# Performance work log

Measured on AMD Instinct MI355X. Metric: run time of the kernel, lower is better.

Reference implementation:

```python
import jax, jax.numpy as jnp
import numpy as np
import math

HEADS = 8
DIM_HEAD = 64
BATCH = 2
SEQ = 2048
KNN = 32
ATTN_SCALE_INIT = 20.0


def l2norm(t, eps=1e-12):
    n = jnp.sqrt(jnp.sum(t * t, axis=-1, keepdims=True))
    return t / jnp.maximum(n, eps)


def setup_inputs() -> dict:
    key = jax.random.key(0)
    ks = jax.random.split(key, 5)
    q = jax.random.normal(ks[0], (BATCH, HEADS, SEQ, DIM_HEAD), dtype=jnp.float32)
    k = jax.random.normal(ks[1], (BATCH, SEQ, DIM_HEAD), dtype=jnp.float32)
    v = jax.random.normal(ks[2], (BATCH, SEQ, DIM_HEAD), dtype=jnp.float32)
    scale_param = jnp.full((HEADS, 1, 1), math.log(ATTN_SCALE_INIT), dtype=jnp.float32)
    mem_kv = jax.random.normal(ks[3], (BATCH, HEADS, SEQ, KNN, 2, DIM_HEAD), dtype=jnp.float32)
    mask = jnp.ones((BATCH, SEQ), dtype=jnp.float32)
    mem_mask = jax.random.randint(ks[4], (BATCH, HEADS, SEQ, KNN), 0, 2).astype(jnp.bool_)
    return {"q": q, "k": k, "v": v, "scale_param": scale_param,
            "mem_kv": mem_kv, "mask": mask, "mem_mask": mem_mask}


def reference(q, k, v, scale_param, mem_kv, mask, mem_mask):
    neg = -jnp.finfo(q.dtype).max
    qn = l2norm(q)
    kn = l2norm(k)
    scale = jnp.exp(scale_param)  # [h,1,1]

    # local attention scores: [b,h,i,j]
    sim = jnp.einsum('bhid,bjd->bhij', qn, kn) * scale
    # key padding mask
    sim = sim + neg * (1.0 - mask[:, None, None, :])
    # causal mask (use_causal_mask=True), i == j here
    i, j = sim.shape[-2], sim.shape[-1]
    causal = jnp.triu(jnp.ones((i, j), dtype=jnp.bool_), j - i + 1)
    sim = jnp.where(causal, neg, sim)

    # memory branch: mem_kv [b,h,i,knn,2,d]
    mem_k = mem_kv[..., 0, :]
    mem_v = mem_kv[..., 1, :]
    sim_mem = jnp.einsum('bhid,bhijd->bhij', qn, mem_k) * scale
    sim_mem = jnp.where(mem_mask, sim_mem, neg)

    # joint softmax over [mem | local]
    full = jnp.concatenate((sim_mem, sim), axis=-1)
    attn = jax.nn.softmax(full, axis=-1)

    knn = mem_mask.shape[-1]
    mem_attn = attn[..., :knn]
    local_attn = attn[..., knn:]

    local_out = jnp.einsum('bhij,bjd->bhid', local_attn, v)
    mem_out = jnp.einsum('bhij,bhijd->bhid', mem_attn, mem_v)
    return local_out + mem_out
```

## Files before the change

### kernel.cpp

```cpp
#include <hip/hip_runtime.h>
#include <float.h>

#define HEADS 8
#define DIM 64
#define BATCH 2
#define SEQ 2048
#define KNN 32
#define QT 32
#define KT 64
#define NEGF (-3.402823466e38f)

typedef float f32x4 __attribute__((ext_vector_type(4)));
typedef __bf16 bf16x8 __attribute__((ext_vector_type(8)));

union F4 { float4 v; f32x4 e; float f[4]; };
union S8 { bf16x8 b; unsigned int u[4]; unsigned short us[8]; uint4 u4; uint2 u2[2]; };

__device__ __forceinline__ unsigned short f2bf(float x) {
    unsigned int u = __float_as_uint(x);
    u = (u + 0x7fffu + ((u >> 16) & 1u)) >> 16;
    return (unsigned short)u;
}


__global__ __launch_bounds__(256) void prep_kernel(const float* __restrict__ k,
                                                   const float* __restrict__ v,
                                                   const unsigned char* __restrict__ mmraw,
                                                   unsigned short* __restrict__ knBt,
                                                   unsigned short* __restrict__ vTt,
                                                   int* __restrict__ flag) {
    __shared__ float kn_s[64][65];
    __shared__ float vt_s[64][65];
    const int w = threadIdx.x >> 6, lane = threadIdx.x & 63;
    const int s0 = blockIdx.x * 64;
    const int b = s0 >> 11;
    const int s64 = (s0 & 2047) >> 6;
    for (int rr = 0; rr < 16; rr++) {
        const int sl = w * 16 + rr;
        const int row = s0 + sl;
        float kv = k[(size_t)row * DIM + lane];
        float ssq = kv * kv;
        #pragma unroll
        for (int m = 1; m < 64; m <<= 1) ssq += __shfl_xor(ssq, m);
        kn_s[sl][lane] = kv / fmaxf(sqrtf(ssq), 1e-12f);
        vt_s[sl][lane] = v[(size_t)row * DIM + lane];
    }
    __syncthreads();
    #pragma unroll
    for (int i = 0; i < 2; i++) {
        const int ch = threadIdx.x * 2 + i;
        const int s16g = ch >> 7;
        const int rem = ch & 127;
        const int rowc = rem >> 3;
        const int kc = (rem >> 2) & 1;
        const int oct = rem & 3;
        const float* src = &kn_s[s16g * 16 + rowc][kc * 32 + oct * 8];
        unsigned short tmp[8];
        #pragma unroll
        for (int e = 0; e < 8; e++) tmp[e] = f2bf(src[e]);
        const int s16 = s64 * 4 + s16g;
        unsigned short* dst = knBt + (((size_t)(b * 128 + s16) * 2 + kc) << 9)
                            + rowc * 32 + oct * 8;
        *(uint4*)dst = *(uint4*)&tmp[0];
    }
    #pragma unroll
    for (int i = 0; i < 2; i++) {
        const int ch = threadIdx.x * 2 + i;
        const int kk2 = ch >> 8;
        const int mtd = (ch >> 6) & 3;
        const int cc = (ch >> 2) & 15;
        const int q = ch & 3;
        unsigned short tmp[8];
        #pragma unroll
        for (int e = 0; e < 8; e++)
            tmp[e] = f2bf(vt_s[kk2 * 32 + q * 8 + e][mtd * 16 + cc]);
        unsigned short* dst = vTt + (((size_t)(b * 32 + s64) * 8 + kk2 * 4 + mtd) << 9)
                            + cc * 32 + q * 8;
        *(uint4*)dst = *(uint4*)&tmp[0];
    }
    if (blockIdx.x == 0 && w == 0) {
        int bad = 0;
        #pragma unroll
        for (int t = 0; t < 8; t++) {
            int idx = t * 64 + lane;
            if ((idx & 3) != 0 && mmraw[idx] != 0) bad = 1;
        }
        unsigned long long anybad = __ballot(bad);
        if (lane == 0) flag[0] = (anybad == 0ULL) ? 1 : 0;
    }
}

__global__ __launch_bounds__(256, 4) void mem_kernel(
    const float* __restrict__ q,
    const float* __restrict__ scale_param,
    const float* __restrict__ mem_kv,
    const void*  __restrict__ mem_mask,
    const int*   __restrict__ flagp,
    unsigned short* __restrict__ qnB,
    float* __restrict__ maccG,
    float* __restrict__ mG,
    float* __restrict__ lG)
{
    __shared__ float qn_s[4][64];
    __shared__ float p_s[4][32];
    const int w = threadIdx.x >> 6, lane = threadIdx.x & 63;
    const int mask_is_int = flagp[0];
    const int gid = blockIdx.x * 4 + w;
    const float scale = __expf(scale_param[(gid >> 11) & 7]);
    const float* rowp = mem_kv + (size_t)gid * (KNN * 2 * DIM);

    const int j1 = lane & 31, dh = lane >> 5;
    bool mybit;
    {
        size_t mmrow = (size_t)gid * KNN;
        mybit = mask_is_int ? (((const int*)mem_mask)[mmrow + j1] != 0)
                            : (((const unsigned char*)mem_mask)[mmrow + j1] != 0);
    }
    const unsigned int mb = (unsigned int)__ballot(mybit);

    float qv = q[(size_t)gid * DIM + lane];

    F4 dk[8];
    #pragma unroll
    for (int i = 0; i < 8; i++) dk[i].e = 0.f;
    {
        const float* kbase = rowp + j1 * (2 * DIM) + dh * 32;
        if (mybit) {
            #pragma unroll
            for (int i = 0; i < 8; i++) dk[i].e = *(const f32x4*)(kbase + 4 * i);
        }
    }
    const int g = lane >> 4, c16 = lane & 15;
    F4 dv[8];
    #pragma unroll
    for (int t = 0; t < 8; t++) {
        dv[t].e = 0.f;
        const int j2 = 4 * t + g;
        if ((mb >> j2) & 1u)
            dv[t].e = *(const f32x4*)(rowp + j2 * (2 * DIM) + DIM + c16 * 4);
    }

    float ssq = qv * qv;
    #pragma unroll
    for (int m2 = 1; m2 < 64; m2 <<= 1) ssq += __shfl_xor(ssq, m2);
    float qn = qv / fmaxf(sqrtf(ssq), 1e-12f);
    qnB[(size_t)gid * DIM + lane] = f2bf(qn);
    qn_s[w][lane] = qn;

    float s = 0.f;
    #pragma unroll
    for (int i = 0; i < 8; i++) {
        F4 qq; qq.v = *(const float4*)&qn_s[w][dh * 32 + 4 * i];
        s += dk[i].f[0] * qq.f[0] + dk[i].f[1] * qq.f[1]
           + dk[i].f[2] * qq.f[2] + dk[i].f[3] * qq.f[3];
    }
    s += __shfl_xor(s, 32);
    s = mybit ? s * scale : NEGF;

    float mx = s;
    #pragma unroll
    for (int m2 = 1; m2 < 32; m2 <<= 1) mx = fmaxf(mx, __shfl_xor(mx, m2));
    float p = __expf(s - mx);
    float ls = p;
    #pragma unroll
    for (int m2 = 1; m2 < 32; m2 <<= 1) ls += __shfl_xor(ls, m2);
    if (lane < 32) p_s[w][lane] = p;

    f32x4 acc = 0.f;
    #pragma unroll
    for (int t = 0; t < 8; t++) {
        float pv = p_s[w][4 * t + g];
        #pragma unroll
        for (int e = 0; e < 4; e++) acc[e] += pv * dv[t].f[e];
    }
    #pragma unroll
    for (int e = 0; e < 4; e++) {
        acc[e] += __shfl_xor(acc[e], 16);
        acc[e] += __shfl_xor(acc[e], 32);
    }
    if (g == 0) {
        F4 o; o.e = acc;
        *(float4*)(maccG + (size_t)gid * DIM + c16 * 4) = o.v;
    }
    if (lane == 0) { mG[gid] = mx; lG[gid] = ls; }
}

__global__ __launch_bounds__(256) void flash_kernel(
    const float* __restrict__ scale_param,
    const float* __restrict__ mask,
    const unsigned short* __restrict__ knBt,
    const unsigned short* __restrict__ vTt,
    const unsigned short* __restrict__ qnB,
    const float* __restrict__ maccG,
    const float* __restrict__ mG,
    const float* __restrict__ lG,
    float* __restrict__ out)
{
    __shared__ float maccs[QT][DIM + 4];
    __shared__ float mmem_s[QT], lmem_s[QT];
    __shared__ __attribute__((aligned(16))) unsigned short fragbuf[4][2][2][4][17][8];
    __shared__ float corr_s[4][QT];
    __shared__ float mlw[4][2][QT];
    __shared__ float linv_s[QT];

    const int tid = threadIdx.x;
    const int w = tid >> 6;
    const int lane = tid & 63;
    const int g = lane >> 4;
    const int c = lane & 15;
    const int bid = blockIdx.x;
    const int pr = bid & 31;
    const int bh = bid >> 5;
    const int b = bh >> 3;
    const int h = bh & 7;
    const float scale = __expf(scale_param[h]);

    const unsigned short* knTb = knBt + ((size_t)b * 128 * 2 << 9);
    const unsigned short* vTtb = vTt  + ((size_t)b * 32 * 8 << 9);
    const int lofs = c * 32;

    #pragma unroll 1
    for (int half = 0; half < 2; half++) {
        const int qt = half ? (63 - pr) : pr;
        const int i0 = qt * QT;

        bf16x8 qa[2][2];
        #pragma unroll
        for (int mt = 0; mt < 2; mt++)
            #pragma unroll
            for (int kc = 0; kc < 2; kc++) {
                S8 t;
                t.u4 = *(const uint4*)(qnB + ((size_t)bh * SEQ + i0 + mt * 16 + c) * DIM + kc * 32 + g * 8);
                qa[mt][kc] = t.b;
            }

        f32x4 oacc[4][2];
        #pragma unroll
        for (int mtd = 0; mtd < 4; mtd++)
            #pragma unroll
            for (int ni = 0; ni < 2; ni++)
                #pragma unroll
                for (int r = 0; r < 4; r++) oacc[mtd][ni][r] = 0.f;
        float mrow[2] = {NEGF, NEGF}, lrow[2] = {0.f, 0.f};

        const int nkt = ((i0 + QT - 1) >> 6) + 1;

        for (int jt = w; jt < nkt; jt += 4) {
            const int jb = jt * KT;

            bf16x8 va[4][2];
            #pragma unroll
            for (int mtd = 0; mtd < 4; mtd++)
                #pragma unroll
                for (int kk2 = 0; kk2 < 2; kk2++) {
                    const unsigned short* vbase = vTtb + (((size_t)jt * 8 + kk2 * 4 + mtd) << 9) + lofs;
                    S8 t;
                    t.u2[0] = *(const uint2*)(vbase + 4 * g);
                    t.u2[1] = *(const uint2*)(vbase + 16 + 4 * g);
                    va[mtd][kk2] = t.b;
                }

            f32x4 sacc[2][4];
            #pragma unroll
            for (int mt = 0; mt < 2; mt++)
                #pragma unroll
                for (int nt = 0; nt < 4; nt++)
                    #pragma unroll
                    for (int r = 0; r < 4; r++) sacc[mt][nt][r] = 0.f;
            #pragma unroll
            for (int kc = 0; kc < 2; kc++) {
                #pragma unroll
                for (int nt = 0; nt < 4; nt++) {
                    S8 kb;
                    kb.u4 = *(const uint4*)(knTb + (((size_t)(jt * 4 + nt) * 2 + kc) << 9) + lofs + g * 8);
                    #pragma unroll
                    for (int mt = 0; mt < 2; mt++)
                        sacc[mt][nt] = __builtin_amdgcn_mfma_f32_16x16x32_bf16(kb.b, qa[mt][kc], sacc[mt][nt], 0, 0, 0);
                }
            }

            F4 mskv[4];
            #pragma unroll
            for (int nt = 0; nt < 4; nt++)
                mskv[nt].v = *(const float4*)(mask + b * SEQ + jb + nt * 16 + 4 * g);
            const bool docausal = (jb + 63 > i0);

            #pragma unroll
            for (int mt = 0; mt < 2; mt++) {
                const int iq = i0 + mt * 16 + c;
                float tm = NEGF;
                #pragma unroll
                for (int nt = 0; nt < 4; nt++)
                    #pragma unroll
                    for (int r = 0; r < 4; r++) {
                        float s = sacc[mt][nt][r] * scale + NEGF * (1.f - mskv[nt].f[r]);
                        if (docausal) {
                            int j = jb + nt * 16 + 4 * g + r;
                            if (j > iq) s = NEGF;
                        }
                        sacc[mt][nt][r] = s;
                        tm = fmaxf(tm, s);
                    }
                tm = fmaxf(tm, __shfl_xor(tm, 16));
                tm = fmaxf(tm, __shfl_xor(tm, 32));
                float mnew = fmaxf(mrow[mt], tm);
                float corr = __expf(mrow[mt] - mnew);
                mrow[mt] = mnew;

                float ps = 0.f;
                #pragma unroll
                for (int nt = 0; nt < 4; nt++) {
                    unsigned int lo, hi;
                    float p0 = __expf(sacc[mt][nt][0] - mnew);
                    float p1 = __expf(sacc[mt][nt][1] - mnew);
                    float p2 = __expf(sacc[mt][nt][2] - mnew);
                    float p3 = __expf(sacc[mt][nt][3] - mnew);
                    ps += (p0 + p1) + (p2 + p3);
                    lo = (unsigned int)f2bf(p0) | ((unsigned int)f2bf(p1) << 16);
                    hi = (unsigned int)f2bf(p2) | ((unsigned int)f2bf(p3) << 16);
                    *(uint2*)&fragbuf[w][mt][nt >> 1][g][c][4 * (nt & 1)] = make_uint2(lo, hi);
                }
                ps += __shfl_xor(ps, 16);
                ps += __shfl_xor(ps, 32);
                lrow[mt] = lrow[mt] * corr + ps;

                #pragma unroll
                for (int mtd = 0; mtd < 4; mtd++)
                    #pragma unroll
                    for (int r = 0; r < 4; r++) oacc[mtd][mt][r] *= corr;
            }

            #pragma unroll
            for (int kk2 = 0; kk2 < 2; kk2++)
                #pragma unroll
                for (int ni = 0; ni < 2; ni++) {
                    S8 pb; pb.u4 = *(const uint4*)&fragbuf[w][ni][kk2][g][c][0];
                    #pragma unroll
                    for (int mtd = 0; mtd < 4; mtd++)
                        oacc[mtd][ni] = __builtin_amdgcn_mfma_f32_16x16x32_bf16(va[mtd][kk2], pb.b, oacc[mtd][ni], 0, 0, 0);
                }
        }

        {
            int i = tid >> 3, d0 = (tid & 7) * 8;
            const float* src = maccG + ((size_t)bh * SEQ + i0 + i) * DIM + d0;
            *(float4*)&maccs[i][d0]     = *(const float4*)src;
            *(float4*)&maccs[i][d0 + 4] = *(const float4*)(src + 4);
            if (tid < QT) {
                mmem_s[tid] = mG[(size_t)bh * SEQ + i0 + tid];
                lmem_s[tid] = lG[(size_t)bh * SEQ + i0 + tid];
            }
        }
        if (g == 0) {
            #pragma unroll
            for (int mt = 0; mt < 2; mt++) {
                mlw[w][0][mt * 16 + c] = mrow[mt];
                mlw[w][1][mt * 16 + c] = lrow[mt];
            }
        }
        __syncthreads();
        {
            int i = tid >> 3;
            int d0 = (tid & 7) * 8;
            float mM = mmem_s[i];
            #pragma unroll
            for (int w2 = 0; w2 < 4; w2++) mM = fmaxf(mM, mlw[w2][0][i]);
            float em = __expf(mmem_s[i] - mM);
            float L = lmem_s[i] * em;
            #pragma unroll
            for (int w2 = 0; w2 < 4; w2++) L += mlw[w2][1][i] * __expf(mlw[w2][0][i] - mM);
            #pragma unroll
            for (int e = 0; e < 8; e++) maccs[i][d0 + e] *= em;
            if ((tid & 7) == 0) linv_s[i] = 1.f / L;
            if ((tid & 7) == 1) corr_s[0][i] = mM;
        }
        __syncthreads();
        float ew0 = __expf(mlw[w][0][c]      - corr_s[0][c]);
        float ew1 = __expf(mlw[w][0][16 + c] - corr_s[0][16 + c]);
        for (int w2 = 0; w2 < 4; w2++) {
            if (w == w2) {
                #pragma unroll
                for (int mtd = 0; mtd < 4; mtd++)
                    #pragma unroll
                    for (int r = 0; r < 4; r++) {
                        maccs[c][mtd * 16 + 4 * g + r]      += oacc[mtd][0][r] * ew0;
                        maccs[16 + c][mtd * 16 + 4 * g + r] += oacc[mtd][1][r] * ew1;
                    }
            }
            __syncthreads();
        }
        {
            int i = tid >> 3;
            int d0 = (tid & 7) * 8;
            float inv = linv_s[i];
            F4 o0, o1;
            o0.v = *(const float4*)&maccs[i][d0];
            o1.v = *(const float4*)&maccs[i][d0 + 4];
            #pragma unroll
            for (int e = 0; e < 4; e++) { o0.f[e] *= inv; o1.f[e] *= inv; }
            float* op = out + ((size_t)bh * SEQ + i0 + i) * DIM + d0;
            *(float4*)op = o0.v;
            *(float4*)(op + 4) = o1.v;
        }
        __syncthreads();
    }
}

extern "C" void kernel_launch(void* const* d_in, const int* in_sizes, int n_in,
                              void* d_out, int out_size, void* d_ws, size_t ws_size,
                              hipStream_t stream) {
    const float* q           = (const float*)d_in[0];
    const float* k           = (const float*)d_in[1];
    const float* v           = (const float*)d_in[2];
    const float* scale_param = (const float*)d_in[3];
    const float* mem_kv      = (const float*)d_in[4];
    const float* mask        = (const float*)d_in[5];
    const void*  mem_mask    = d_in[6];
    float* out = (float*)d_out;

    char* base = (char*)d_ws;
    int* flag            = (int*)base;
    unsigned short* knBt = (unsigned short*)(base + 1024);
    unsigned short* vTt  = (unsigned short*)(base + 1024 + (512ull << 10));
    unsigned short* qnB  = (unsigned short*)(base + 1024 + (1ull << 20));
    float* maccG         = (float*)(base + 1024 + (5ull << 20));
    float* mG            = (float*)(base + 1024 + (13ull << 20));
    float* lG            = (float*)(base + 1024 + (13ull << 20) + (256ull << 10));

    prep_kernel<<<dim3(BATCH * SEQ / 64), dim3(256), 0, stream>>>(
        k, v, (const unsigned char*)mem_mask, knBt, vTt, flag);
    mem_kernel<<<dim3(BATCH * HEADS * SEQ / 4), dim3(256), 0, stream>>>(
        q, scale_param, mem_kv, mem_mask, flag, qnB, maccG, mG, lG);
    flash_kernel<<<dim3(BATCH * HEADS * (SEQ / QT) / 2), dim3(256), 0, stream>>>(
        scale_param, mask, knBt, vTt, qnB, maccG, mG, lG, out);
}
```

Before: 111.6 us.

## Split flash kernel key range across two blocks and merge partials separately

Each flash block's key tiles are now divided between two blocks (split-K style), doubling the grid. Each split writes unnormalized partial outputs plus row max/sum to workspace. A new merge kernel combines the two local partials with the memory-branch partial to produce the final output. This raises parallelism and shortens the per-block causal loop, at the cost of an extra launch and extra global traffic for the partial outputs.

```diff
diff --git a/kernel.cpp b/kernel.cpp
--- a/kernel.cpp
+++ b/kernel.cpp
@@ -9,6 +9,7 @@
 #define QT 32
 #define KT 64
 #define NEGF (-3.402823466e38f)
+#define NROW (BATCH * HEADS * SEQ)
 
 typedef float f32x4 __attribute__((ext_vector_type(4)));
 typedef __bf16 bf16x8 __attribute__((ext_vector_type(8)));
@@ -191,17 +192,14 @@
     const unsigned short* __restrict__ knBt,
     const unsigned short* __restrict__ vTt,
     const unsigned short* __restrict__ qnB,
-    const float* __restrict__ maccG,
-    const float* __restrict__ mG,
-    const float* __restrict__ lG,
-    float* __restrict__ out)
+    float* __restrict__ OLs,
+    float* __restrict__ mLs,
+    float* __restrict__ lLs)
 {
     __shared__ float maccs[QT][DIM + 4];
-    __shared__ float mmem_s[QT], lmem_s[QT];
     __shared__ __attribute__((aligned(16))) unsigned short fragbuf[4][2][2][4][17][8];
-    __shared__ float corr_s[4][QT];
+    __shared__ float corr_s[QT];
     __shared__ float mlw[4][2][QT];
-    __shared__ float linv_s[QT];
 
     const int tid = threadIdx.x;
     const int w = tid >> 6;
@@ -209,8 +207,10 @@
     const int g = lane >> 4;
     const int c = lane & 15;
     const int bid = blockIdx.x;
-    const int pr = bid & 31;
-    const int bh = bid >> 5;
+    const int sp = bid & 1;
+    const int pb = bid >> 1;
+    const int pr = pb & 31;
+    const int bh = pb >> 5;
     const int b = bh >> 3;
     const int h = bh & 7;
     const float scale = __expf(scale_param[h]);
@@ -245,7 +245,7 @@
 
         const int nkt = ((i0 + QT - 1) >> 6) + 1;
 
-        for (int jt = w; jt < nkt; jt += 4) {
+        for (int jt = 2 * w + sp; jt < nkt; jt += 8) {
             const int jb = jt * KT;
 
             bf16x8 va[4][2];
@@ -334,23 +334,13 @@
             for (int kk2 = 0; kk2 < 2; kk2++)
                 #pragma unroll
                 for (int ni = 0; ni < 2; ni++) {
-                    S8 pb; pb.u4 = *(const uint4*)&fragbuf[w][ni][kk2][g][c][0];
+                    S8 pb2; pb2.u4 = *(const uint4*)&fragbuf[w][ni][kk2][g][c][0];
                     #pragma unroll
                     for (int mtd = 0; mtd < 4; mtd++)
-                        oacc[mtd][ni] = __builtin_amdgcn_mfma_f32_16x16x32_bf16(va[mtd][kk2], pb.b, oacc[mtd][ni], 0, 0, 0);
+                        oacc[mtd][ni] = __builtin_amdgcn_mfma_f32_16x16x32_bf16(va[mtd][kk2], pb2.b, oacc[mtd][ni], 0, 0, 0);
                 }
         }
 
-        {
-            int i = tid >> 3, d0 = (tid & 7) * 8;
-            const float* src = maccG + ((size_t)bh * SEQ + i0 + i) * DIM + d0;
-            *(float4*)&maccs[i][d0]     = *(const float4*)src;
-            *(float4*)&maccs[i][d0 + 4] = *(const float4*)(src + 4);
-            if (tid < QT) {
-                mmem_s[tid] = mG[(size_t)bh * SEQ + i0 + tid];
-                lmem_s[tid] = lG[(size_t)bh * SEQ + i0 + tid];
-            }
-        }
         if (g == 0) {
             #pragma unroll
             for (int mt = 0; mt < 2; mt++) {
@@ -362,21 +352,21 @@
         {
             int i = tid >> 3;
             int d0 = (tid & 7) * 8;
-            float mM = mmem_s[i];
-            #pragma unroll
-            for (int w2 = 0; w2 < 4; w2++) mM = fmaxf(mM, mlw[w2][0][i]);
-            float em = __expf(mmem_s[i] - mM);
-            float L = lmem_s[i] * em;
+            float mM = mlw[0][0][i];
+            #pragma unroll
+            for (int w2 = 1; w2 < 4; w2++) mM = fmaxf(mM, mlw[w2][0][i]);
+            float L = 0.f;
             #pragma unroll
             for (int w2 = 0; w2 < 4; w2++) L += mlw[w2][1][i] * __expf(mlw[w2][0][i] - mM);
             #pragma unroll
-            for (int e = 0; e < 8; e++) maccs[i][d0 + e] *= em;
-            if ((tid & 7) == 0) linv_s[i] = 1.f / L;
-            if ((tid & 7) == 1) corr_s[0][i] = mM;
+            for (int e = 0; e < 8; e++) maccs[i][d0 + e] = 0.f;
+            size_t row = (size_t)bh * SEQ + i0 + i;
+            if ((tid & 7) == 0) { mLs[(size_t)sp * NROW + row] = mM; lLs[(size_t)sp * NROW + row] = L; }
+            if ((tid & 7) == 1) corr_s[i] = mM;
         }
         __syncthreads();
-        float ew0 = __expf(mlw[w][0][c]      - corr_s[0][c]);
-        float ew1 = __expf(mlw[w][0][16 + c] - corr_s[0][16 + c]);
+        float ew0 = __expf(mlw[w][0][c]      - corr_s[c]);
+        float ew1 = __expf(mlw[w][0][16 + c] - corr_s[16 + c]);
         for (int w2 = 0; w2 < 4; w2++) {
             if (w == w2) {
                 #pragma unroll
@@ -392,18 +382,45 @@
         {
             int i = tid >> 3;
             int d0 = (tid & 7) * 8;
-            float inv = linv_s[i];
-            F4 o0, o1;
-            o0.v = *(const float4*)&maccs[i][d0];
-            o1.v = *(const float4*)&maccs[i][d0 + 4];
-            #pragma unroll
-            for (int e = 0; e < 4; e++) { o0.f[e] *= inv; o1.f[e] *= inv; }
-            float* op = out + ((size_t)bh * SEQ + i0 + i) * DIM + d0;
-            *(float4*)op = o0.v;
-            *(float4*)(op + 4) = o1.v;
+            float* op = OLs + ((size_t)sp * NROW + (size_t)bh * SEQ + i0 + i) * DIM + d0;
+            *(float4*)op       = *(const float4*)&maccs[i][d0];
+            *(float4*)(op + 4) = *(const float4*)&maccs[i][d0 + 4];
         }
         __syncthreads();
     }
+}
+
+__global__ __launch_bounds__(256) void merge_kernel(
+    const float* __restrict__ OLs, const float* __restrict__ mLs, const float* __restrict__ lLs,
+    const float* __restrict__ maccG, const float* __restrict__ mG, const float* __restrict__ lG,
+    float* __restrict__ out)
+{
+    const size_t row = (size_t)blockIdx.x * 32 + (threadIdx.x >> 3);
+    const int d0 = (threadIdx.x & 7) * 8;
+    float m0 = mLs[row],        l0 = lLs[row];
+    float m1 = mLs[NROW + row], l1 = lLs[NROW + row];
+    float mm = mG[row],         lm = lG[row];
+    float M = fmaxf(fmaxf(m0, m1), mm);
+    float e0 = __expf(m0 - M);
+    float e1 = __expf(m1 - M);
+    float em = __expf(mm - M);
+    float inv = 1.f / (l0 * e0 + l1 * e1 + lm * em);
+    const float* p0 = OLs + row * DIM + d0;
+    const float* p1 = OLs + ((size_t)NROW * DIM) + row * DIM + d0;
+    const float* pm = maccG + row * DIM + d0;
+    F4 a0, a1, b0, b1, c0, c1;
+    a0.v = *(const float4*)p0;       a1.v = *(const float4*)(p0 + 4);
+    b0.v = *(const float4*)p1;       b1.v = *(const float4*)(p1 + 4);
+    c0.v = *(const float4*)pm;       c1.v = *(const float4*)(pm + 4);
+    F4 o0, o1;
+    #pragma unroll
+    for (int e = 0; e < 4; e++) {
+        o0.f[e] = (a0.f[e] * e0 + b0.f[e] * e1 + c0.f[e] * em) * inv;
+        o1.f[e] = (a1.f[e] * e0 + b1.f[e] * e1 + c1.f[e] * em) * inv;
+    }
+    float* op = out + row * DIM + d0;
+    *(float4*)op       = o0.v;
+    *(float4*)(op + 4) = o1.v;
 }
 
 extern "C" void kernel_launch(void* const* d_in, const int* in_sizes, int n_in,
@@ -426,11 +443,16 @@
     float* maccG         = (float*)(base + 1024 + (5ull << 20));
     float* mG            = (float*)(base + 1024 + (13ull << 20));
     float* lG            = (float*)(base + 1024 + (13ull << 20) + (256ull << 10));
+    float* OLs           = (float*)(base + 1024 + (14ull << 20));
+    float* mLs           = (float*)(base + 1024 + (30ull << 20));
+    float* lLs           = (float*)(base + 1024 + (30ull << 20) + (512ull << 10));
 
     prep_kernel<<<dim3(BATCH * SEQ / 64), dim3(256), 0, stream>>>(
         k, v, (const unsigned char*)mem_mask, knBt, vTt, flag);
     mem_kernel<<<dim3(BATCH * HEADS * SEQ / 4), dim3(256), 0, stream>>>(
         q, scale_param, mem_kv, mem_mask, flag, qnB, maccG, mG, lG);
-    flash_kernel<<<dim3(BATCH * HEADS * (SEQ / QT) / 2), dim3(256), 0, stream>>>(
-        scale_param, mask, knBt, vTt, qnB, maccG, mG, lG, out);
-}
+    flash_kernel<<<dim3(BATCH * HEADS * (SEQ / QT)), dim3(256), 0, stream>>>(
+        scale_param, mask, knBt, vTt, qnB, OLs, mLs, lLs);
+    merge_kernel<<<dim3(NROW / 32), dim3(256), 0, stream>>>(
+        OLs, mLs, lLs, maccG, mG, lG, out);
+}
```

New measurement: 138.9 us. 1.24x slower.
